# Kernel optimization log

Measured on AMD Instinct MI355X. Metric: run time of the kernel, lower is better.

The kernel has to match this reference:

```python
import jax, jax.numpy as jnp
import numpy as np

B, NM, NB, Z, H, K = 1024, 20000, 25000, 64, 256, 20
BETA = 0.1
LOG2PI = float(np.log(2.0 * np.pi))


def _log_normal(x, m, v):
    D = x.shape[-1]
    return (-0.5 * D * LOG2PI
            - 0.5 * jnp.sum(jnp.log(v), axis=-1)
            - 0.5 * jnp.sum((x - m) ** 2 / v, axis=-1))


def _kl_gmm(z, q_m, q_logv, p_m, p_logv):
    log_q = _log_normal(z, q_m, jnp.exp(q_logv))                               # [B]
    lp = _log_normal(z[:, None, :], p_m[None], jnp.exp(p_logv)[None])          # [B,K]
    log_p = jax.scipy.special.logsumexp(lp, axis=1) - jnp.log(float(p_m.shape[0]))
    return jnp.sum(log_q - log_p)


def _dist2(x, y):
    # ||x_i - y_j||_2^2, expanded form (avoids the [R,C,D] broadcast of the torch code)
    x2 = jnp.sum(x * x, axis=1, keepdims=True)
    y2 = jnp.sum(y * y, axis=1, keepdims=True)
    return x2 + y2.T - 2.0 * (x @ y.T)


def _distance_gmm(mu_s, mu_d, lv_s, lv_d):
    return _dist2(mu_s, mu_d) + _dist2(jnp.exp(0.5 * lv_s), jnp.exp(0.5 * lv_d)) + 1e-6


def _cost_mat(cost_s, cost_t, tran):
    f1 = jnp.sum(cost_s ** 2, axis=1, keepdims=True) / cost_s.shape[0]  # [ns,1]
    f2 = jnp.sum(cost_t ** 2, axis=1, keepdims=True) / cost_t.shape[0]  # [nt,1]
    return f1 + f2.T - 2.0 * (cost_s @ tran @ cost_t.T)


def _fgw(mu, z_mu, logvar, z_logvar):
    c_post = _distance_gmm(mu, mu, logvar, logvar)
    c_prior = _distance_gmm(z_mu, z_mu, z_logvar, z_logvar)
    c_pp = _distance_gmm(mu, z_mu, logvar, z_logvar)
    ns, nt = c_post.shape[0], c_prior.shape[0]
    p_s = jnp.ones((ns, 1), c_post.dtype) / ns
    p_t = jnp.ones((nt, 1), c_post.dtype) / nt

    def compute_tran(c_post, c_prior, c_pp):
        def outer(carry, _):
            tran, dual = carry
            cost = BETA * _cost_mat(c_post, c_prior, tran) + (1.0 - BETA) * c_pp
            kernel = jnp.exp(-cost / jnp.max(jnp.abs(cost))) * tran
            b = p_t / (kernel.T @ dual)

            def inner(c2, _):
                dual, b = c2
                dual = p_s / (kernel @ b)
                b = p_t / (kernel.T @ dual)
                return (dual, b), None

            (dual, b), _ = jax.lax.scan(inner, (dual, b), None, length=5)
            tran = (dual @ b.T) * kernel
            return (tran, dual), None

        init = (jnp.ones((ns, nt), c_post.dtype) / (ns * nt),
                jnp.ones((ns, 1), c_post.dtype) / ns)
        (tran, _), _ = jax.lax.scan(outer, init, None, length=10)
        return jnp.where(jnp.any(jnp.isnan(tran)),
                         jnp.ones((ns, nt), tran.dtype) / (ns * nt), tran)

    # torch detaches tran before the final cost, so cut all gradient through the loop
    tran = jax.lax.stop_gradient(compute_tran(c_post, c_prior, c_pp))
    cost = BETA * _cost_mat(c_post, c_prior, tran) + (1.0 - BETA) * c_pp
    return jnp.sum(cost * tran)


def _forward(batch_user_x, batch_user_y, p_mu_a, p_logv_a, p_mu_b, p_logv_b,
             eps_x, eps_y, eps_xr, eps_yr,
             W1a, b1a, W21a, b21a, W22a, b22a, W3a, b3a, W4a, b4a,
             W1b, b1b, W21b, b21b, W22b, b22b, W3b, b3b, W4b, b4b):
    def enc_a(x):
        h = jax.nn.relu(x @ W1a + b1a)
        return h @ W21a + b21a, h @ W22a + b22a

    def dec_a(z):
        return jax.nn.relu(z @ W3a + b3a) @ W4a + b4a

    def enc_b(x):
        h = jax.nn.relu(x @ W1b + b1b)
        return h @ W21b + b21b, h @ W22b + b22b

    def dec_b(z):
        return jax.nn.relu(z @ W3b + b3b) @ W4b + b4b

    # dropout rate = 0.0 -> identity
    mu_a, logvar_a = enc_a(batch_user_x)
    z_x = mu_a + eps_x * jnp.exp(0.5 * logvar_a)
    preds_x = dec_a(z_x)
    mu_b, logvar_b = enc_b(batch_user_y)
    z_y = mu_b + eps_y * jnp.exp(0.5 * logvar_b)
    preds_y = dec_b(z_y)

    gmm_reg_loss_a = _kl_gmm(z_x, mu_a, logvar_a, p_mu_a, p_logv_a)
    gmm_reg_loss_b = _kl_gmm(z_y, mu_b, logvar_b, p_mu_b, p_logv_b)
    align_global_loss = _fgw(mu_b, mu_a, logvar_b, logvar_a)

    preds_x2y = dec_b(z_x)
    preds_y2x = dec_a(z_y)
    m_xr, lv_xr = enc_b(preds_x2y)
    feature_x_r = m_xr + eps_xr * jnp.exp(0.5 * lv_xr)
    m_yr, lv_yr = enc_a(preds_y2x)
    feature_y_r = m_yr + eps_yr * jnp.exp(0.5 * lv_yr)

    cyc_loss_x = jnp.linalg.norm(z_x - feature_x_r)
    cyc_loss_y = jnp.linalg.norm(z_y - feature_y_r)
    return (preds_x, preds_y, preds_x2y, preds_y2x, z_x, z_y,
            gmm_reg_loss_a, gmm_reg_loss_b, feature_x_r, feature_y_r,
            align_global_loss, cyc_loss_x, cyc_loss_y)


def setup_inputs() -> dict:
    key = jax.random.key(0)
    ks = jax.random.split(key, 24)

    def nrm(i, shape, s=1.0):
        return jax.random.normal(ks[i], shape, dtype=jnp.float32) * s

    return {
        "user_1": jax.random.randint(ks[0], (B,), 0, 100000),
        "user_2": jax.random.randint(ks[1], (B,), 0, 100000),
        "batch_user_x": jax.random.uniform(ks[2], (B, NM), dtype=jnp.float32),
        "batch_user_y": jax.random.uniform(ks[3], (B, NB), dtype=jnp.float32),
        "p_mu_a": nrm(4, (K, Z)), "p_logv_a": nrm(5, (K, Z), 0.1),
        "p_mu_b": nrm(6, (K, Z)), "p_logv_b": nrm(7, (K, Z), 0.1),
        "eps_x": nrm(8, (B, Z)), "eps_y": nrm(9, (B, Z)),
        "eps_xr": nrm(10, (B, Z)), "eps_yr": nrm(11, (B, Z)),
        "W1a": nrm(12, (NM, H), 0.02), "b1a": jnp.zeros((H,), jnp.float32),
        "W21a": nrm(13, (H, Z), 0.02), "b21a": jnp.zeros((Z,), jnp.float32),
        "W22a": nrm(14, (H, Z), 0.02), "b22a": jnp.zeros((Z,), jnp.float32),
        "W3a": nrm(15, (Z, H), 0.02), "b3a": jnp.zeros((H,), jnp.float32),
        "W4a": nrm(16, (H, NM), 0.02), "b4a": jnp.zeros((NM,), jnp.float32),
        "W1b": nrm(17, (NB, H), 0.02), "b1b": jnp.zeros((H,), jnp.float32),
        "W21b": nrm(18, (H, Z), 0.02), "b21b": jnp.zeros((Z,), jnp.float32),
        "W22b": nrm(19, (H, Z), 0.02), "b22b": jnp.zeros((Z,), jnp.float32),
        "W3b": nrm(20, (Z, H), 0.02), "b3b": jnp.zeros((H,), jnp.float32),
        "W4b": nrm(21, (H, NB), 0.02), "b4b": jnp.zeros((NB,), jnp.float32),
    }


def reference(user_1, user_2, batch_user_x, batch_user_y, p_mu_a, p_logv_a, p_mu_b, p_logv_b,
              eps_x, eps_y, eps_xr, eps_yr,
              W1a, b1a, W21a, b21a, W22a, b22a, W3a, b3a, W4a, b4a,
              W1b, b1b, W21b, b21b, W22b, b22b, W3b, b3b, W4b, b4b):
    # user_1/user_2 are unused by the torch forward as well
    return _forward(batch_user_x, batch_user_y, p_mu_a, p_logv_a, p_mu_b, p_logv_b,
                    eps_x, eps_y, eps_xr, eps_yr,
                    W1a, b1a, W21a, b21a, W22a, b22a, W3a, b3a, W4a, b4a,
                    W1b, b1b, W21b, b21b, W22b, b22b, W3b, b3b, W4b, b4b)
```

## Files before the change

### kernel.cpp

```cpp
#include <hip/hip_runtime.h>


#define DEVI __device__ __forceinline__

typedef __attribute__((ext_vector_type(4))) float  f32x4;
typedef __attribute__((ext_vector_type(4))) short  s16x4;
typedef __attribute__((ext_vector_type(8))) short  s16x8;
typedef __attribute__((ext_vector_type(8))) __bf16 bf16x8;

DEVI short f2bf(float f) {
  unsigned u = __float_as_uint(f);
  u += 0x7fffu + ((u >> 16) & 1u);
  return (short)(u >> 16);
}
DEVI float bf2f(unsigned short u) { return __uint_as_float(((unsigned)u) << 16); }

DEVI f32x4 mfma16(bf16x8 a, bf16x8 b, f32x4 c) {
  return __builtin_amdgcn_mfma_f32_16x16x32_bf16(a, b, c, 0, 0, 0);
}

struct GemmArgs {
  const float* Af;
  const unsigned short* Bt;
  float* outF;
  const float* bias;
  float* partials;
  int M, N, K;
  int lda, ldbt, ldc;
  int totSteps, nSplits;
};

enum { EPI_PARTIAL, EPI_BIAS, EPI_BF16, EPI_COST, EPI_LOSS };

template<int BM, int BN, int WR, int WC, int EPI>
DEVI void gemm_body(const GemmArgs g)
{
  constexpr int BK = 64, BKP = 72;
  constexpr int NT = WR * WC * 64;
  __shared__ short As[BM * BKP];
  __shared__ short Bs[BN * BKP];

  const int m0 = blockIdx.x * BM;
  int n0 = 0, kb0 = 0, kb1 = g.K, split = 0;
  if constexpr (EPI == EPI_PARTIAL) {
    split = blockIdx.y;
    int s0 = (split * g.totSteps) / g.nSplits;
    int s1 = ((split + 1) * g.totSteps) / g.nSplits;
    kb0 = s0 * BK;
    kb1 = s1 * BK; if (kb1 > g.K) kb1 = g.K;
  } else {
    n0 = blockIdx.y * BN;
  }
  const int tid  = threadIdx.x;
  const int lane = tid & 63;
  const int wv   = tid >> 6;
  const int wr   = wv % WR;
  const int wc   = wv / WR;

  f32x4 acc[2][4];
  #pragma unroll
  for (int i = 0; i < 2; ++i)
    #pragma unroll
    for (int j = 0; j < 4; ++j) acc[i][j] = f32x4{0.f, 0.f, 0.f, 0.f};

  for (int kb = kb0; kb < kb1; kb += BK) {
    {
      constexpr int NV = BM * BK / 4;
      #pragma unroll
      for (int i = 0; i < NV / NT; ++i) {
        int idx = tid + NT * i;
        int r = idx >> 4, q = idx & 15;
        int k = kb + 4 * q;
        f32x4 v = f32x4{0.f, 0.f, 0.f, 0.f};
        if (k < kb1) v = *(const f32x4*)(g.Af + (size_t)(m0 + r) * g.lda + k);
        s16x4 s;
        s.x = f2bf(v.x); s.y = f2bf(v.y); s.z = f2bf(v.z); s.w = f2bf(v.w);
        *(s16x4*)&As[r * BKP + 4 * q] = s;
      }
    }
    {
      constexpr int NV = BN * BK / 8;
      #pragma unroll
      for (int i = 0; i < NV / NT; ++i) {
        int idx = tid + NT * i;
        int r = idx >> 3, q = idx & 7;
        int k = kb + 8 * q;
        s16x8 v{};
        if ((n0 + r) < g.N && k < kb1)
          v = *(const s16x8*)(g.Bt + (size_t)(n0 + r) * g.ldbt + k);
        *(s16x8*)&Bs[r * BKP + 8 * q] = v;
      }
    }
    __syncthreads();
    #pragma unroll
    for (int s = 0; s < 2; ++s) {
      const int ko = 32 * s + 8 * (lane >> 4);
      bf16x8 a0 = *(const bf16x8*)&As[(wr * 32 +      (lane & 15)) * BKP + ko];
      bf16x8 a1 = *(const bf16x8*)&As[(wr * 32 + 16 + (lane & 15)) * BKP + ko];
      #pragma unroll
      for (int fn = 0; fn < 4; ++fn) {
        bf16x8 b = *(const bf16x8*)&Bs[(wc * 64 + fn * 16 + (lane & 15)) * BKP + ko];
        acc[0][fn] = mfma16(a0, b, acc[0][fn]);
        acc[1][fn] = mfma16(a1, b, acc[1][fn]);
      }
    }
    __syncthreads();
  }

  #pragma unroll
  for (int fm = 0; fm < 2; ++fm) {
    #pragma unroll
    for (int fn = 0; fn < 4; ++fn) {
      #pragma unroll
      for (int p = 0; p < 4; ++p) {
        int gm = m0 + wr * 32 + fm * 16 + (lane >> 4) * 4 + p;
        int gn = n0 + wc * 64 + fn * 16 + (lane & 15);
        float v = acc[fm][fn][p];
        if constexpr (EPI == EPI_PARTIAL) {
          g.partials[((size_t)split * g.M + gm) * 256 + gn] = v;
        } else {
          if (gn < g.N) g.outF[(size_t)gm * g.ldc + gn] = v + g.bias[gn];
        }
      }
    }
  }
}

template<int BM, int BN, int WR, int WC, int EPI>
__global__ __launch_bounds__(WR*WC*64)
void k_gemm2(GemmArgs g0, GemmArgs g1)
{
  gemm_body<BM, BN, WR, WC, EPI>(blockIdx.z ? g1 : g0);
}

struct FgwGemmArgs {
  const unsigned short* A;
  const unsigned short* Bt;
  unsigned short* U;
  float* cost;
  const float* f1;
  const float* f2;
  const float* cpp;
  const float* tran;
  unsigned* mx;
  float* loss;
  float* braw;
};

template<int EPI>
__global__ __launch_bounds__(256)
void k_fgw_gemm(FgwGemmArgs a)
{
  __shared__ short As[64 * 72];
  __shared__ short Bs[64 * 72];
  __shared__ float red[4];

  const int bid = blockIdx.x, tid = threadIdx.x;
  const int lane = tid & 63, wv = tid >> 6;
  const int wr = wv & 1, wc = wv >> 1;
  const int m0 = (bid >> 4) * 64, n0 = (bid & 15) * 64;

  if constexpr (EPI == EPI_COST) {
    if (bid == 0) {
      #pragma unroll
      for (int i = 0; i < 4; ++i) a.braw[tid + 256 * i] = 0.f;
    }
  }

  f32x4 acc[2][2];
  #pragma unroll
  for (int i = 0; i < 2; ++i)
    #pragma unroll
    for (int j = 0; j < 2; ++j) acc[i][j] = f32x4{0.f, 0.f, 0.f, 0.f};

  for (int kb = 0; kb < 1024; kb += 64) {
    #pragma unroll
    for (int i = 0; i < 2; ++i) {
      int idx = tid + 256 * i;
      int r = idx >> 3, q = idx & 7;
      *(s16x8*)&As[r * 72 + 8 * q] = *(const s16x8*)&a.A [(size_t)(m0 + r) * 1024 + kb + 8 * q];
      *(s16x8*)&Bs[r * 72 + 8 * q] = *(const s16x8*)&a.Bt[(size_t)(n0 + r) * 1024 + kb + 8 * q];
    }
    __syncthreads();
    #pragma unroll
    for (int s = 0; s < 2; ++s) {
      const int ko = 32 * s + 8 * (lane >> 4);
      bf16x8 a0 = *(const bf16x8*)&As[(wr * 32 +      (lane & 15)) * 72 + ko];
      bf16x8 a1 = *(const bf16x8*)&As[(wr * 32 + 16 + (lane & 15)) * 72 + ko];
      bf16x8 b0 = *(const bf16x8*)&Bs[(wc * 32 +      (lane & 15)) * 72 + ko];
      bf16x8 b1 = *(const bf16x8*)&Bs[(wc * 32 + 16 + (lane & 15)) * 72 + ko];
      acc[0][0] = mfma16(a0, b0, acc[0][0]);
      acc[1][0] = mfma16(a1, b0, acc[1][0]);
      acc[0][1] = mfma16(a0, b1, acc[0][1]);
      acc[1][1] = mfma16(a1, b1, acc[1][1]);
    }
    __syncthreads();
  }

  float lred = 0.f;
  #pragma unroll
  for (int fm = 0; fm < 2; ++fm) {
    #pragma unroll
    for (int fn = 0; fn < 2; ++fn) {
      #pragma unroll
      for (int p = 0; p < 4; ++p) {
        int gm = m0 + wr * 32 + fm * 16 + (lane >> 4) * 4 + p;
        int gn = n0 + wc * 32 + fn * 16 + (lane & 15);
        float v = acc[fm][fn][p];
        size_t o = (size_t)gm * 1024 + gn;
        if constexpr (EPI == EPI_BF16) {
          a.U[o] = (unsigned short)f2bf(v);
        } else {
          float c = 0.1f * (a.f1[gm] + a.f2[gn] - 2.f * v) + 0.9f * a.cpp[o];
          if constexpr (EPI == EPI_COST) {
            a.cost[o] = c;
            lred = fmaxf(lred, fabsf(c));
          } else {
            lred += c * a.tran[o];
          }
        }
      }
    }
  }
  if constexpr (EPI != EPI_BF16) {
    #pragma unroll
    for (int off = 32; off; off >>= 1) {
      float t = __shfl_xor(lred, off, 64);
      lred = (EPI == EPI_COST) ? fmaxf(lred, t) : (lred + t);
    }
    if (lane == 0) red[wv] = lred;
    __syncthreads();
    if (tid == 0) {
      if constexpr (EPI == EPI_COST) {
        float t = fmaxf(fmaxf(red[0], red[1]), fmaxf(red[2], red[3]));
        atomicMax(a.mx, __float_as_uint(t));
      } else {
        atomicAdd(a.loss, red[0] + red[1] + red[2] + red[3]);
      }
    }
  }
}

struct FP {
  const float* mu[2]; const float* lv[2];
  unsigned short* F[2]; float* n[2];
};
__global__ __launch_bounds__(64)
void k_featprep(FP a)
{
  const int y = blockIdx.y;
  const int i = blockIdx.x;
  const int t = threadIdx.x;
  float v0 = a.mu[y][(size_t)i * 64 + t];
  float v1 = expf(0.5f * a.lv[y][(size_t)i * 64 + t]);
  unsigned short u0 = (unsigned short)f2bf(v0);
  unsigned short u1 = (unsigned short)f2bf(v1);
  unsigned short* Fr = a.F[y] + (size_t)i * 128;
  Fr[t] = u0;
  Fr[64 + t] = u1;
  float r0 = bf2f(u0), r1 = bf2f(u1);
  float p = r0 * r0 + r1 * r1;
  #pragma unroll
  for (int o = 32; o; o >>= 1) p += __shfl_xor(p, o, 64);
  if (t == 0) a.n[y][i] = p;
}

struct DistMMArgs {
  const unsigned short* Fx[3]; const unsigned short* Fy[3];
  const float* nx[3]; const float* ny[3];
  unsigned short* outB[2]; float* outF; float* frow[2];
};
__global__ __launch_bounds__(256)
void k_distmm(DistMMArgs a)
{
  __shared__ short As[64 * 72];
  __shared__ short Bs[64 * 72];
  const int z = blockIdx.y;
  const int bid = blockIdx.x, tid = threadIdx.x;
  const int lane = tid & 63, wv = tid >> 6;
  const int wr = wv & 1, wc = wv >> 1;
  const int m0 = (bid >> 4) * 64, n0 = (bid & 15) * 64;
  const unsigned short* X = a.Fx[z];
  const unsigned short* Y = a.Fy[z];

  f32x4 acc[2][2];
  #pragma unroll
  for (int i = 0; i < 2; ++i)
    #pragma unroll
    for (int j = 0; j < 2; ++j) acc[i][j] = f32x4{0.f, 0.f, 0.f, 0.f};

  #pragma unroll
  for (int kb = 0; kb < 128; kb += 64) {
    #pragma unroll
    for (int i = 0; i < 2; ++i) {
      int idx = tid + 256 * i;
      int r = idx >> 3, q = idx & 7;
      *(s16x8*)&As[r * 72 + 8 * q] = *(const s16x8*)&X[(size_t)(m0 + r) * 128 + kb + 8 * q];
      *(s16x8*)&Bs[r * 72 + 8 * q] = *(const s16x8*)&Y[(size_t)(n0 + r) * 128 + kb + 8 * q];
    }
    __syncthreads();
    #pragma unroll
    for (int s = 0; s < 2; ++s) {
      const int ko = 32 * s + 8 * (lane >> 4);
      bf16x8 a0 = *(const bf16x8*)&As[(wr * 32 +      (lane & 15)) * 72 + ko];
      bf16x8 a1 = *(const bf16x8*)&As[(wr * 32 + 16 + (lane & 15)) * 72 + ko];
      bf16x8 b0 = *(const bf16x8*)&Bs[(wc * 32 +      (lane & 15)) * 72 + ko];
      bf16x8 b1 = *(const bf16x8*)&Bs[(wc * 32 + 16 + (lane & 15)) * 72 + ko];
      acc[0][0] = mfma16(a0, b0, acc[0][0]);
      acc[1][0] = mfma16(a1, b0, acc[1][0]);
      acc[0][1] = mfma16(a0, b1, acc[0][1]);
      acc[1][1] = mfma16(a1, b1, acc[1][1]);
    }
    __syncthreads();
  }

  const float* nxp = a.nx[z];
  const float* nyp = a.ny[z];
  float rp[2][4];
  #pragma unroll
  for (int fm = 0; fm < 2; ++fm)
    #pragma unroll
    for (int p = 0; p < 4; ++p) rp[fm][p] = 0.f;

  #pragma unroll
  for (int fm = 0; fm < 2; ++fm) {
    #pragma unroll
    for (int fn = 0; fn < 2; ++fn) {
      #pragma unroll
      for (int p = 0; p < 4; ++p) {
        int gm = m0 + wr * 32 + fm * 16 + (lane >> 4) * 4 + p;
        int gn = n0 + wc * 32 + fn * 16 + (lane & 15);
        float val = nxp[gm] + nyp[gn] - 2.f * acc[fm][fn][p] + 1e-6f;
        if (z == 2) a.outF[(size_t)gm * 1024 + gn] = val;
        else {
          a.outB[z][(size_t)gm * 1024 + gn] = (unsigned short)f2bf(val);
          rp[fm][p] += val * val;
        }
      }
    }
  }
  if (z < 2) {
    #pragma unroll
    for (int fm = 0; fm < 2; ++fm)
      #pragma unroll
      for (int p = 0; p < 4; ++p) {
        float v = rp[fm][p];
        v += __shfl_xor(v, 1, 64);
        v += __shfl_xor(v, 2, 64);
        v += __shfl_xor(v, 4, 64);
        v += __shfl_xor(v, 8, 64);
        rp[fm][p] = v;
      }
    if ((lane & 15) == 0) {
      #pragma unroll
      for (int fm = 0; fm < 2; ++fm)
        #pragma unroll
        for (int p = 0; p < 4; ++p) {
          int gm = m0 + wr * 32 + fm * 16 + (lane >> 4) * 4 + p;
          atomicAdd(&a.frow[z][gm], rp[fm][p] * (1.f / 1024.f));
        }
    }
  }
}

__global__ __launch_bounds__(256)
void k_kbuild(const float* cost, const float* tran, const unsigned* mxbits,
              const float* draw, float* braw, float* K, float* KT)
{
  __shared__ float t[64 * 65];
  __shared__ float dualS[64];
  __shared__ float csum[4][64];
  const int r0 = blockIdx.x * 64, c0 = blockIdx.y * 64;
  const int tid = threadIdx.x;
  const float inv = 1.f / __uint_as_float(*mxbits);
  const float PS = 1.f / 1024.f;
  if (tid < 64) dualS[tid] = PS / draw[r0 + tid];
  __syncthreads();
  float colpart = 0.f;
  #pragma unroll
  for (int i = 0; i < 16; ++i) {
    int idx = tid + 256 * i;
    int r = idx >> 6, c = idx & 63;
    size_t o = (size_t)(r0 + r) * 1024 + (c0 + c);
    float v = expf(-cost[o] * inv) * tran[o];
    K[o] = v;
    t[r * 65 + c] = v;
    colpart += v * dualS[r];
  }
  csum[tid >> 6][tid & 63] = colpart;
  __syncthreads();
  #pragma unroll
  for (int i = 0; i < 16; ++i) {
    int idx = tid + 256 * i;
    int c = idx >> 6, r = idx & 63;
    KT[(size_t)(c0 + c) * 1024 + (r0 + r)] = t[r * 65 + c];
  }
  if (tid < 64)
    atomicAdd(&braw[c0 + tid],
              csum[0][tid] + csum[1][tid] + csum[2][tid] + csum[3][tid]);
}

__global__ __launch_bounds__(256)
void k_matvec(const float* M, const float* xraw, float* yraw)
{
  const int r = blockIdx.x * 4 + (threadIdx.x >> 6);
  const int lane = threadIdx.x & 63;
  const float C = 1.f / 1024.f;
  const f32x4* row = (const f32x4*)(M + (size_t)r * 1024);
  const f32x4* xv  = (const f32x4*)xraw;
  float s = 0.f;
  #pragma unroll
  for (int q = 0; q < 4; ++q) {
    f32x4 a = row[lane + 64 * q];
    f32x4 x = xv [lane + 64 * q];
    s += a.x * (C / x.x) + a.y * (C / x.y) + a.z * (C / x.z) + a.w * (C / x.w);
  }
  #pragma unroll
  for (int o = 32; o; o >>= 1) s += __shfl_xor(s, o, 64);
  if (lane == 0) yraw[r] = s;
}

__global__ __launch_bounds__(256)
void k_tranupd(const float* K, const float* draw, const float* braw,
               float* tran, unsigned short* tranT, unsigned* flag, int check)
{
  __shared__ float t[64 * 65];
  __shared__ float dualS[64], bS[64];
  const int r0 = blockIdx.x * 64, c0 = blockIdx.y * 64;
  const int tid = threadIdx.x;
  const float P = 1.f / 1024.f;
  if (tid < 64) dualS[tid] = P / draw[r0 + tid];
  else if (tid < 128) bS[tid - 64] = P / braw[c0 + tid - 64];
  __syncthreads();
  unsigned bad = 0;
  #pragma unroll
  for (int i = 0; i < 16; ++i) {
    int idx = tid + 256 * i;
    int r = idx >> 6, c = idx & 63;
    size_t o = (size_t)(r0 + r) * 1024 + (c0 + c);
    float v = dualS[r] * bS[c] * K[o];
    tran[o] = v;
    t[r * 65 + c] = v;
    if (v != v) bad = 1u;
  }
  __syncthreads();
  #pragma unroll
  for (int i = 0; i < 16; ++i) {
    int idx = tid + 256 * i;
    int c = idx >> 6, r = idx & 63;
    tranT[(size_t)(c0 + c) * 1024 + (r0 + r)] = (unsigned short)f2bf(t[r * 65 + c]);
  }
  if (check && bad) atomicOr(flag, 1u);
}

struct T4 { const float* in[4]; unsigned short* out[4]; int R[4], C[4], nx[4], nt[4]; };
__global__ void k_transpose4(T4 d)
{
  __shared__ float t[64][65];
  const int z = blockIdx.y;
  const int tile = blockIdx.x;
  if (tile >= d.nt[z]) return;
  const int R = d.R[z], C = d.C[z];
  const int r0 = (tile % d.nx[z]) * 64, c0 = (tile / d.nx[z]) * 64;
  const float* in = d.in[z];
  unsigned short* out = d.out[z];
  const int tid = threadIdx.x;
  #pragma unroll
  for (int i = 0; i < 16; ++i) {
    int idx = tid + 256 * i;
    int r = idx >> 6, c = idx & 63;
    float v = 0.f;
    if ((r0 + r) < R && (c0 + c) < C) v = in[(size_t)(r0 + r) * C + (c0 + c)];
    t[r][c] = v;
  }
  __syncthreads();
  #pragma unroll
  for (int i = 0; i < 16; ++i) {
    int idx = tid + 256 * i;
    int c = idx >> 6, r = idx & 63;
    if ((c0 + c) < C && (r0 + r) < R)
      out[(size_t)(c0 + c) * R + (r0 + r)] = (unsigned short)f2bf(t[r][c]);
  }
}

__global__ void k_wcomb_reduce(const float* partials, unsigned short* WcTa,
                               unsigned short* WcTb)
{
  __shared__ float t[64][65];
  const int z = blockIdx.z;
  const float* P = partials + (size_t)z * 32 * 256 * 256;
  unsigned short* WcT = z ? WcTb : WcTa;
  const int u0 = blockIdx.x * 64, v0 = blockIdx.y * 64;
  const int tid = threadIdx.x;
  #pragma unroll
  for (int i = 0; i < 16; ++i) {
    int idx = tid + 256 * i;
    int u = idx >> 6, v = idx & 63;
    float s = 0.f;
    for (int p = 0; p < 32; ++p)
      s += P[(size_t)p * 65536 + (u0 + u) * 256 + (v0 + v)];
    t[u][v] = s;
  }
  __syncthreads();
  #pragma unroll
  for (int i = 0; i < 16; ++i) {
    int idx = tid + 256 * i;
    int v = idx >> 6, u = idx & 63;
    WcT[(size_t)(v0 + v) * 256 + (u0 + u)] = (unsigned short)f2bf(t[u][v]);
  }
}

struct BcArgs {
  const float* b4[2]; const unsigned short* Wt1[2]; const float* b1[2];
  float* bc[2]; int K[2];
};
__global__ void k_bcvec(BcArgs a)
{
  const int y = blockIdx.y;
  const int c = blockIdx.x * 4 + (threadIdx.x >> 6);
  const int lane = threadIdx.x & 63;
  const int K = a.K[y];
  const unsigned short* wrow = a.Wt1[y] + (size_t)c * K;
  const float* b4 = a.b4[y];
  float s = 0.f;
  for (int k = lane * 8; k < K; k += 512) {
    s16x8 w = *(const s16x8*)&wrow[k];
    f32x4 v0 = *(const f32x4*)&b4[k];
    f32x4 v1 = *(const f32x4*)&b4[k + 4];
    s += v0.x * bf2f((unsigned short)w[0]) + v0.y * bf2f((unsigned short)w[1])
       + v0.z * bf2f((unsigned short)w[2]) + v0.w * bf2f((unsigned short)w[3])
       + v1.x * bf2f((unsigned short)w[4]) + v1.y * bf2f((unsigned short)w[5])
       + v1.z * bf2f((unsigned short)w[6]) + v1.w * bf2f((unsigned short)w[7]);
  }
  #pragma unroll
  for (int o = 32; o; o >>= 1) s += __shfl_xor(s, o, 64);
  if (lane == 0) a.bc[y][c] = s + a.b1[y][c];
}

struct Red2 { const float* partials[2]; const float* bias[2]; float* h[2]; int ns; };
__global__ void k_reduce2(Red2 a)
{
  const int y = blockIdx.y;
  int idx = blockIdx.x * 256 + threadIdx.x;
  float s = a.bias[y][idx & 255];
  const float* P = a.partials[y];
  for (int p = 0; p < a.ns; ++p) s += P[(size_t)p * (1024 * 256) + idx];
  a.h[y][idx] = fmaxf(s, 0.f);
}

struct EH2 {
  const float* h[2]; const float* W21[2]; const float* b21[2];
  const float* W22[2]; const float* b22[2]; const float* eps[2];
  float* mu[2]; float* lv[2]; float* zO[2];
};
__global__ void k_enc_head2(EH2 a)
{
  __shared__ float hrow[256];
  __shared__ float res[128];
  const int y = blockIdx.y;
  const int i = blockIdx.x;
  const int t = threadIdx.x;
  hrow[t]       = a.h[y][(size_t)i * 256 + t];
  hrow[t + 128] = a.h[y][(size_t)i * 256 + t + 128];
  __syncthreads();
  const int c = t & 63;
  const float* W = (t < 64) ? a.W21[y] : a.W22[y];
  float acc = (t < 64) ? a.b21[y][c] : a.b22[y][c];
  #pragma unroll 8
  for (int j = 0; j < 256; ++j) acc += hrow[j] * W[j * 64 + c];
  res[t] = acc;
  __syncthreads();
  if (t < 64) {
    float mu = res[t], lv = res[64 + t];
    a.mu[y][(size_t)i * 64 + t] = mu;
    a.lv[y][(size_t)i * 64 + t] = lv;
    a.zO[y][(size_t)i * 64 + t] = mu + a.eps[y][(size_t)i * 64 + t] * expf(0.5f * lv);
  }
}

struct RencArgs {
  const float* hd[2]; const unsigned short* WcT[2]; const float* bc[2];
  const float* W21[2]; const float* b21[2]; const float* W22[2]; const float* b22[2];
  const float* eps[2]; float* fout[2];
};
__global__ void k_renc_head(RencArgs a)
{
  __shared__ float hdrow[256];
  __shared__ float hr[256];
  __shared__ float res[128];
  const int y = blockIdx.y;
  const int i = blockIdx.x;
  const int t = threadIdx.x;
  hdrow[t] = a.hd[y][(size_t)i * 256 + t];
  __syncthreads();
  {
    const s16x8* wr = (const s16x8*)(a.WcT[y] + (size_t)t * 256);
    float s = a.bc[y][t];
    #pragma unroll 4
    for (int j = 0; j < 32; ++j) {
      s16x8 w = wr[j];
      const float* hp = &hdrow[j * 8];
      s += hp[0] * bf2f((unsigned short)w[0]) + hp[1] * bf2f((unsigned short)w[1])
         + hp[2] * bf2f((unsigned short)w[2]) + hp[3] * bf2f((unsigned short)w[3])
         + hp[4] * bf2f((unsigned short)w[4]) + hp[5] * bf2f((unsigned short)w[5])
         + hp[6] * bf2f((unsigned short)w[6]) + hp[7] * bf2f((unsigned short)w[7]);
    }
    hr[t] = fmaxf(s, 0.f);
  }
  __syncthreads();
  if (t < 128) {
    const int c = t & 63;
    const float* W = (t < 64) ? a.W21[y] : a.W22[y];
    float acc = (t < 64) ? a.b21[y][c] : a.b22[y][c];
    #pragma unroll 8
    for (int j = 0; j < 256; ++j) acc += hr[j] * W[j * 64 + c];
    res[t] = acc;
  }
  __syncthreads();
  if (t < 64) {
    float mu = res[t], lv = res[64 + t];
    a.fout[y][(size_t)i * 64 + t] = mu + a.eps[y][(size_t)i * 64 + t] * expf(0.5f * lv);
  }
}

struct DH4 { const float* z[4]; const float* W3[4]; const float* b3[4]; float* hd[4]; };
__global__ void k_dec_head4(DH4 a)
{
  __shared__ float zrow[64];
  const int y = blockIdx.y;
  const int i = blockIdx.x;
  const int t = threadIdx.x;
  if (t < 64) zrow[t] = a.z[y][(size_t)i * 64 + t];
  __syncthreads();
  const float* W3 = a.W3[y];
  float acc = a.b3[y][t];
  #pragma unroll
  for (int d = 0; d < 64; ++d) acc += zrow[d] * W3[d * 256 + t];
  a.hd[y][(size_t)i * 256 + t] = fmaxf(acc, 0.f);
}

__global__ void k_init(float* tran, unsigned short* tranT, float* draw, float* braw,
                       float* f1, float* f2, unsigned* mx, unsigned* nanflag,
                       float* cyc, float* ga, float* gb, float* al)
{
  const int bid = blockIdx.x, tid = threadIdx.x;
  const float v = 1.f / (1024.f * 1024.f);
  const unsigned short vb = (unsigned short)f2bf(v);
  const size_t base = (size_t)bid * 1024;
  #pragma unroll
  for (int i = 0; i < 4; ++i) {
    tran [base + tid + 256 * i] = v;
    tranT[base + tid + 256 * i] = vb;
  }
  if (bid == 0) {
    #pragma unroll
    for (int i = 0; i < 4; ++i) {
      int k = tid + 256 * i;
      draw[k] = 1.f; braw[k] = 0.f; f1[k] = 0.f; f2[k] = 0.f;
    }
    if (tid < 16) mx[tid] = 0u;
    if (tid == 0) { *nanflag = 0u; cyc[0] = 0.f; cyc[1] = 0.f; *ga = 0.f; *gb = 0.f; *al = 0.f; }
  }
}

__global__ void k_nanfix(float* tran, unsigned short* tranT, const unsigned* flag)
{
  if (*flag == 0u) return;
  const int bid = blockIdx.x, tid = threadIdx.x;
  const float v = 1.f / (1024.f * 1024.f);
  const unsigned short vb = (unsigned short)f2bf(v);
  const size_t base = (size_t)bid * 1024;
  #pragma unroll
  for (int i = 0; i < 4; ++i) {
    tran [base + tid + 256 * i] = v;
    tranT[base + tid + 256 * i] = vb;
  }
}

struct G2 {
  const float* z[2]; const float* mu[2]; const float* lv[2];
  const float* pmu[2]; const float* plv[2]; float* o[2];
};
__global__ void k_gmm2(G2 a)
{
  const int y = blockIdx.y;
  const int i = blockIdx.x;
  const int d = threadIdx.x;
  const float zd = a.z[y][(size_t)i * 64 + d];
  const float m  = a.mu[y][(size_t)i * 64 + d];
  const float l  = a.lv[y][(size_t)i * 64 + d];
  float t = l + (zd - m) * (zd - m) * expf(-l);
  #pragma unroll
  for (int o = 32; o; o >>= 1) t += __shfl_xor(t, o, 64);
  const float C0 = 64.f * 1.8378770664093453f;
  float logq = -0.5f * (C0 + t);
  float lp[20];
  #pragma unroll
  for (int k = 0; k < 20; ++k) {
    float pm = a.pmu[y][k * 64 + d], pl = a.plv[y][k * 64 + d];
    float u = pl + (zd - pm) * (zd - pm) * expf(-pl);
    #pragma unroll
    for (int o = 32; o; o >>= 1) u += __shfl_xor(u, o, 64);
    lp[k] = -0.5f * (C0 + u);
  }
  float mx = lp[0];
  #pragma unroll
  for (int k = 1; k < 20; ++k) mx = fmaxf(mx, lp[k]);
  float s = 0.f;
  #pragma unroll
  for (int k = 0; k < 20; ++k) s += expf(lp[k] - mx);
  float logp = mx + logf(s) - 2.9957322735539909f;
  if (d == 0) atomicAdd(a.o[y], logq - logp);
}

struct Sq2 { const float* a[2]; const float* b[2]; float* cyc; };
__global__ void k_sqdiff2(Sq2 g)
{
  __shared__ float red[4];
  const int y = blockIdx.y;
  int idx = blockIdx.x * 256 + threadIdx.x;
  float d = g.a[y][idx] - g.b[y][idx];
  d = d * d;
  #pragma unroll
  for (int o = 32; o; o >>= 1) d += __shfl_xor(d, o, 64);
  int lane = threadIdx.x & 63, wv = threadIdx.x >> 6;
  if (lane == 0) red[wv] = d;
  __syncthreads();
  if (threadIdx.x == 0) atomicAdd(g.cyc + y, red[0] + red[1] + red[2] + red[3]);
}

__global__ void k_finish(const float* slots, float* o1, float* o2)
{
  if (threadIdx.x == 0) { *o1 = sqrtf(slots[0]); *o2 = sqrtf(slots[1]); }
}

extern "C" void kernel_launch(void* const* d_in, const int* in_sizes, int n_in,
                              void* d_out, int out_size, void* d_ws, size_t ws_size,
                              hipStream_t stream)
{
  (void)in_sizes; (void)n_in; (void)out_size; (void)ws_size;

  const float* X     = (const float*)d_in[2];
  const float* Y     = (const float*)d_in[3];
  const float* pmua  = (const float*)d_in[4];
  const float* plva  = (const float*)d_in[5];
  const float* pmub  = (const float*)d_in[6];
  const float* plvb  = (const float*)d_in[7];
  const float* epsx  = (const float*)d_in[8];
  const float* epsy  = (const float*)d_in[9];
  const float* epsxr = (const float*)d_in[10];
  const float* epsyr = (const float*)d_in[11];
  const float* W1a = (const float*)d_in[12];  const float* b1a = (const float*)d_in[13];
  const float* W21a= (const float*)d_in[14];  const float* b21a= (const float*)d_in[15];
  const float* W22a= (const float*)d_in[16];  const float* b22a= (const float*)d_in[17];
  const float* W3a = (const float*)d_in[18];  const float* b3a = (const float*)d_in[19];
  const float* W4a = (const float*)d_in[20];  const float* b4a = (const float*)d_in[21];
  const float* W1b = (const float*)d_in[22];  const float* b1b = (const float*)d_in[23];
  const float* W21b= (const float*)d_in[24];  const float* b21b= (const float*)d_in[25];
  const float* W22b= (const float*)d_in[26];  const float* b22b= (const float*)d_in[27];
  const float* W3b = (const float*)d_in[28];  const float* b3b = (const float*)d_in[29];
  const float* W4b = (const float*)d_in[30];  const float* b4b = (const float*)d_in[31];

  float* out = (float*)d_out;
  const size_t P_X = 0, P_Y = 20480000, P_X2Y = 46080000, P_Y2X = 71680000;
  const size_t Z_X = 92160000, Z_Y = 92225536;
  const size_t GMM_A = 92291072, GMM_B = 92291073;
  const size_t F_XR = 92291074, F_YR = 92356610;
  const size_t ALIGN = 92422146, CYC_X = 92422147, CYC_Y = 92422148;

  char* w = (char*)d_ws;
  size_t off = 0;
  auto alloc = [&](size_t bytes) -> void* {
    void* p = w + off;
    off += (bytes + 255) & ~(size_t)255;
    return p;
  };
  unsigned short* Wt1a = (unsigned short*)alloc((size_t)256 * 20000 * 2);
  unsigned short* Wt1b = (unsigned short*)alloc((size_t)256 * 25000 * 2);
  unsigned short* W4ta = (unsigned short*)alloc((size_t)20000 * 256 * 2);
  unsigned short* W4tb = (unsigned short*)alloc((size_t)25000 * 256 * 2);
  unsigned short* WcTa = (unsigned short*)alloc((size_t)256 * 256 * 2);
  unsigned short* WcTb = (unsigned short*)alloc((size_t)256 * 256 * 2);
  float* bca  = (float*)alloc(256 * 4);
  float* bcb  = (float*)alloc(256 * 4);
  float* h0   = (float*)alloc((size_t)1024 * 256 * 4);
  float* h1   = (float*)alloc((size_t)1024 * 256 * 4);
  float* mu_a = (float*)alloc(1024 * 64 * 4);
  float* lv_a = (float*)alloc(1024 * 64 * 4);
  float* mu_b = (float*)alloc(1024 * 64 * 4);
  float* lv_b = (float*)alloc(1024 * 64 * 4);
  float* f1   = (float*)alloc(1024 * 4);
  float* f2   = (float*)alloc(1024 * 4);
  unsigned* mx      = (unsigned*)alloc(16 * 4);
  unsigned* nanflag = (unsigned*)alloc(256);
  float* cyc  = (float*)alloc(256);
  float* draw = (float*)alloc(1024 * 4);
  float* braw = (float*)alloc(1024 * 4);
  unsigned short* Fb = (unsigned short*)alloc((size_t)1024 * 128 * 2);
  unsigned short* Fa = (unsigned short*)alloc((size_t)1024 * 128 * 2);
  float* nb = (float*)alloc(1024 * 4);
  float* na = (float*)alloc(1024 * 4);
  char* arena = (char*)alloc((size_t)32 * 1024 * 1024);
  float* partials = (float*)arena;
  size_t ao = 0;
  auto aalloc = [&](size_t bytes) -> void* {
    void* p = arena + ao;
    ao += (bytes + 255) & ~(size_t)255;
    return p;
  };
  unsigned short* cpostB  = (unsigned short*)aalloc((size_t)1024 * 1024 * 2);
  unsigned short* cpriorB = (unsigned short*)aalloc((size_t)1024 * 1024 * 2);
  float* cpp  = (float*)aalloc((size_t)1024 * 1024 * 4);
  float* tran = (float*)aalloc((size_t)1024 * 1024 * 4);
  unsigned short* tranT = (unsigned short*)aalloc((size_t)1024 * 1024 * 2);
  unsigned short* Umat  = (unsigned short*)aalloc((size_t)1024 * 1024 * 2);
  float* cost  = (float*)aalloc((size_t)1024 * 1024 * 4);
  float* Kmat  = (float*)aalloc((size_t)1024 * 1024 * 4);
  float* KTmat = (float*)aalloc((size_t)1024 * 1024 * 4);
  float* hd0 = (float*)(arena);
  float* hd1 = (float*)(arena + (size_t)1024 * 256 * 4);
  float* hd2 = (float*)(arena + (size_t)2 * 1024 * 256 * 4);
  float* hd3 = (float*)(arena + (size_t)3 * 1024 * 256 * 4);

  {
    T4 d{};
    d.in[0] = W1a; d.out[0] = Wt1a; d.R[0] = 20000; d.C[0] = 256;
    d.in[1] = W1b; d.out[1] = Wt1b; d.R[1] = 25000; d.C[1] = 256;
    d.in[2] = W4a; d.out[2] = W4ta; d.R[2] = 256;   d.C[2] = 20000;
    d.in[3] = W4b; d.out[3] = W4tb; d.R[3] = 256;   d.C[3] = 25000;
    for (int z = 0; z < 4; ++z) {
      d.nx[z] = (d.R[z] + 63) / 64;
      d.nt[z] = d.nx[z] * ((d.C[z] + 63) / 64);
    }
    k_transpose4<<<dim3(1564, 4), 256, 0, stream>>>(d);
  }

  k_init<<<1024, 256, 0, stream>>>(tran, tranT, draw, braw, f1, f2, mx, nanflag,
                                   cyc, out + GMM_A, out + GMM_B, out + ALIGN);

  {
    GemmArgs ga{}, gb{};
    ga.Af = W4a; ga.Bt = Wt1a; ga.partials = partials;
    ga.M = 256; ga.N = 256; ga.K = 20000; ga.lda = 20000; ga.ldbt = 20000;
    ga.totSteps = 313; ga.nSplits = 32;
    gb = ga;
    gb.Af = W4b; gb.Bt = Wt1b; gb.partials = partials + (size_t)32 * 65536;
    gb.K = 25000; gb.lda = 25000; gb.ldbt = 25000; gb.totSteps = 391;
    k_gemm2<128, 256, 4, 4, EPI_PARTIAL><<<dim3(2, 32, 2), 1024, 0, stream>>>(ga, gb);
    k_wcomb_reduce<<<dim3(4, 4, 2), 256, 0, stream>>>(partials, WcTa, WcTb);
    BcArgs bc{};
    bc.b4[0] = b4a; bc.Wt1[0] = Wt1a; bc.b1[0] = b1a; bc.bc[0] = bca; bc.K[0] = 20000;
    bc.b4[1] = b4b; bc.Wt1[1] = Wt1b; bc.b1[1] = b1b; bc.bc[1] = bcb; bc.K[1] = 25000;
    k_bcvec<<<dim3(64, 2), 256, 0, stream>>>(bc);
  }

  {
    GemmArgs ga{}, gb{};
    ga.Af = X; ga.Bt = Wt1a; ga.partials = partials;
    ga.M = 1024; ga.N = 256; ga.K = 20000; ga.lda = 20000; ga.ldbt = 20000;
    ga.totSteps = 313; ga.nSplits = 16;
    gb = ga;
    gb.Af = Y; gb.Bt = Wt1b; gb.partials = partials + (size_t)16 * 1024 * 256;
    gb.K = 25000; gb.lda = 25000; gb.ldbt = 25000; gb.totSteps = 391;
    k_gemm2<128, 256, 4, 4, EPI_PARTIAL><<<dim3(8, 16, 2), 1024, 0, stream>>>(ga, gb);
    Red2 r{};
    r.partials[0] = partials; r.partials[1] = partials + (size_t)16 * 1024 * 256;
    r.bias[0] = b1a; r.bias[1] = b1b; r.h[0] = h0; r.h[1] = h1; r.ns = 16;
    k_reduce2<<<dim3(1024, 2), 256, 0, stream>>>(r);
    EH2 e{};
    e.h[0] = h0; e.W21[0] = W21a; e.b21[0] = b21a; e.W22[0] = W22a; e.b22[0] = b22a;
    e.eps[0] = epsx; e.mu[0] = mu_a; e.lv[0] = lv_a; e.zO[0] = out + Z_X;
    e.h[1] = h1; e.W21[1] = W21b; e.b21[1] = b21b; e.W22[1] = W22b; e.b22[1] = b22b;
    e.eps[1] = epsy; e.mu[1] = mu_b; e.lv[1] = lv_b; e.zO[1] = out + Z_Y;
    k_enc_head2<<<dim3(1024, 2), 128, 0, stream>>>(e);
  }

  {
    G2 g{};
    g.z[0] = out + Z_X; g.mu[0] = mu_a; g.lv[0] = lv_a; g.pmu[0] = pmua; g.plv[0] = plva;
    g.o[0] = out + GMM_A;
    g.z[1] = out + Z_Y; g.mu[1] = mu_b; g.lv[1] = lv_b; g.pmu[1] = pmub; g.plv[1] = plvb;
    g.o[1] = out + GMM_B;
    k_gmm2<<<dim3(1024, 2), 64, 0, stream>>>(g);
  }

  {
    FP fp{};
    fp.mu[0] = mu_b; fp.lv[0] = lv_b; fp.F[0] = Fb; fp.n[0] = nb;
    fp.mu[1] = mu_a; fp.lv[1] = lv_a; fp.F[1] = Fa; fp.n[1] = na;
    k_featprep<<<dim3(1024, 2), 64, 0, stream>>>(fp);
    DistMMArgs dm{};
    dm.Fx[0] = Fb; dm.Fy[0] = Fb; dm.nx[0] = nb; dm.ny[0] = nb;
    dm.Fx[1] = Fa; dm.Fy[1] = Fa; dm.nx[1] = na; dm.ny[1] = na;
    dm.Fx[2] = Fb; dm.Fy[2] = Fa; dm.nx[2] = nb; dm.ny[2] = na;
    dm.outB[0] = cpostB; dm.outB[1] = cpriorB; dm.outF = cpp;
    dm.frow[0] = f1; dm.frow[1] = f2;
    k_distmm<<<dim3(256, 3), 256, 0, stream>>>(dm);
  }
  FgwGemmArgs fg{};
  fg.f1 = f1; fg.f2 = f2; fg.cpp = cpp; fg.loss = out + ALIGN; fg.braw = braw;
  for (int it = 0; it < 10; ++it) {
    fg.A = cpostB; fg.Bt = tranT; fg.U = Umat;
    k_fgw_gemm<EPI_BF16><<<256, 256, 0, stream>>>(fg);
    fg.A = Umat; fg.Bt = cpriorB; fg.cost = cost; fg.mx = mx + it;
    k_fgw_gemm<EPI_COST><<<256, 256, 0, stream>>>(fg);
    k_kbuild<<<dim3(16, 16), 256, 0, stream>>>(cost, tran, mx + it, draw, braw, Kmat, KTmat);
    for (int r = 0; r < 5; ++r) {
      k_matvec<<<256, 256, 0, stream>>>(Kmat,  braw, draw);
      k_matvec<<<256, 256, 0, stream>>>(KTmat, draw, braw);
    }
    k_tranupd<<<dim3(16, 16), 256, 0, stream>>>(Kmat, draw, braw, tran, tranT,
                                                nanflag, it == 9 ? 1 : 0);
  }
  k_nanfix<<<1024, 256, 0, stream>>>(tran, tranT, nanflag);
  fg.A = cpostB; fg.Bt = tranT; fg.U = Umat;
  k_fgw_gemm<EPI_BF16><<<256, 256, 0, stream>>>(fg);
  fg.A = Umat; fg.Bt = cpriorB; fg.tran = tran;
  k_fgw_gemm<EPI_LOSS><<<256, 256, 0, stream>>>(fg);

  {
    DH4 d{};
    d.z[0] = out + Z_X; d.W3[0] = W3a; d.b3[0] = b3a; d.hd[0] = hd0;
    d.z[1] = out + Z_Y; d.W3[1] = W3a; d.b3[1] = b3a; d.hd[1] = hd1;
    d.z[2] = out + Z_Y; d.W3[2] = W3b; d.b3[2] = b3b; d.hd[2] = hd2;
    d.z[3] = out + Z_X; d.W3[3] = W3b; d.b3[3] = b3b; d.hd[3] = hd3;
    k_dec_head4<<<dim3(1024, 4), 256, 0, stream>>>(d);
  }

  {
    RencArgs r{};
    r.hd[0] = hd3; r.WcT[0] = WcTb; r.bc[0] = bcb;
    r.W21[0] = W21b; r.b21[0] = b21b; r.W22[0] = W22b; r.b22[0] = b22b;
    r.eps[0] = epsxr; r.fout[0] = out + F_XR;
    r.hd[1] = hd1; r.WcT[1] = WcTa; r.bc[1] = bca;
    r.W21[1] = W21a; r.b21[1] = b21a; r.W22[1] = W22a; r.b22[1] = b22a;
    r.eps[1] = epsyr; r.fout[1] = out + F_YR;
    k_renc_head<<<dim3(1024, 2), 256, 0, stream>>>(r);
  }

  {
    Sq2 s{};
    s.a[0] = out + Z_X; s.b[0] = out + F_XR;
    s.a[1] = out + Z_Y; s.b[1] = out + F_YR;
    s.cyc = cyc;
    k_sqdiff2<<<dim3(256, 2), 256, 0, stream>>>(s);
    k_finish<<<1, 64, 0, stream>>>(cyc, out + CYC_X, out + CYC_Y);
  }

  {
    GemmArgs ga{}, gb{};
    ga.Af = hd0; ga.Bt = W4ta; ga.outF = out + P_X; ga.bias = b4a;
    ga.M = 1024; ga.N = 20000; ga.K = 256; ga.lda = 256; ga.ldbt = 256; ga.ldc = 20000;
    gb = ga; gb.Af = hd1; gb.outF = out + P_Y2X;
    k_gemm2<128, 256, 4, 4, EPI_BIAS><<<dim3(8, 79, 2), 1024, 0, stream>>>(ga, gb);

    GemmArgs gc{}, gd{};
    gc.Af = hd2; gc.Bt = W4tb; gc.outF = out + P_Y; gc.bias = b4b;
    gc.M = 1024; gc.N = 25000; gc.K = 256; gc.lda = 256; gc.ldbt = 256; gc.ldc = 25000;
    gd = gc; gd.Af = hd3; gd.outF = out + P_X2Y;
    k_gemm2<128, 256, 4, 4, EPI_BIAS><<<dim3(8, 98, 2), 1024, 0, stream>>>(gc, gd);
  }
}
```

Before: 1.549 ms.

## Fuse Sinkhorn kernel build, matvecs and transport update into one persistent kernel

Replaces the per-iteration sequence of k_kbuild, ten k_matvec launches and k_tranupd with a single k_sinkhorn kernel. It runs 16 blocks of 1024 threads, each owning 64 rows, and uses software grid barriers built on atomic counters between phases. The aim is to remove about a dozen launches and their inter-kernel gaps per outer iteration, and to precompute the reciprocal dual vector once in shared memory. The trade-off is that only 16 CUs do all the memory-bound K/KT build, matvec and update work. Correctness also depends on the spin barriers and on cross-CU visibility of K, KT, draw and braw.

```diff
diff --git a/kernel.cpp b/kernel.cpp
--- a/kernel.cpp
+++ b/kernel.cpp
@@ -241,6 +241,142 @@
   }
 }
 
+#define SB 16
+
+struct SinkArgs {
+  const float* cost; const float* tran; const unsigned* mx;
+  float* K; float* KT;
+  float* draw; float* braw;
+  float* tranO; unsigned short* tranTO;
+  unsigned* cnt; unsigned* nanflag; int check;
+};
+
+DEVI void gbar(unsigned* c)
+{
+  __threadfence();
+  __syncthreads();
+  if (threadIdx.x == 0) {
+    __hip_atomic_fetch_add(c, 1u, __ATOMIC_ACQ_REL, __HIP_MEMORY_SCOPE_AGENT);
+    while (__hip_atomic_load(c, __ATOMIC_ACQUIRE, __HIP_MEMORY_SCOPE_AGENT) < (unsigned)SB)
+      __builtin_amdgcn_s_sleep(1);
+  }
+  __syncthreads();
+  __threadfence();
+}
+
+DEVI void mvp(const float* M, const float* x, float* y, int r0, float* invx)
+{
+  const int tid = threadIdx.x;
+  invx[tid] = (1.f / 1024.f) / x[tid];
+  __syncthreads();
+  const int wv = tid >> 6, lane = tid & 63;
+  #pragma unroll
+  for (int pass = 0; pass < 4; ++pass) {
+    const int r = r0 + pass * 16 + wv;
+    const f32x4* row = (const f32x4*)(M + (size_t)r * 1024);
+    float s = 0.f;
+    #pragma unroll
+    for (int q = 0; q < 4; ++q) {
+      f32x4 av = row[lane + 64 * q];
+      f32x4 iv = *(const f32x4*)&invx[4 * (lane + 64 * q)];
+      s += av.x * iv.x + av.y * iv.y + av.z * iv.z + av.w * iv.w;
+    }
+    #pragma unroll
+    for (int o = 32; o; o >>= 1) s += __shfl_xor(s, o, 64);
+    if (lane == 0) y[r] = s;
+  }
+  __syncthreads();
+}
+
+__global__ __launch_bounds__(1024)
+void k_sinkhorn(SinkArgs a)
+{
+  __shared__ float tt[64 * 65];
+  __shared__ float dS[64];
+  __shared__ float csum[16][64];
+  __shared__ float invx[1024];
+
+  const int bid = blockIdx.x, tid = threadIdx.x;
+  const int r0 = bid * 64;
+  const float PS = 1.f / 1024.f;
+  const float inv = 1.f / __uint_as_float(*a.mx);
+
+  if (tid < 64) dS[tid] = PS / a.draw[r0 + tid];
+  __syncthreads();
+
+  for (int jt = 0; jt < 16; ++jt) {
+    const int c0 = jt * 64;
+    float colp = 0.f;
+    #pragma unroll
+    for (int i = 0; i < 4; ++i) {
+      int idx = tid + 1024 * i;
+      int r = idx >> 6, c = idx & 63;
+      size_t o = (size_t)(r0 + r) * 1024 + c0 + c;
+      float v = expf(-a.cost[o] * inv) * a.tran[o];
+      a.K[o] = v;
+      tt[r * 65 + c] = v;
+      colp += v * dS[r];
+    }
+    csum[tid >> 6][tid & 63] = colp;
+    __syncthreads();
+    #pragma unroll
+    for (int i = 0; i < 4; ++i) {
+      int idx = tid + 1024 * i;
+      int c = idx >> 6, r = idx & 63;
+      a.KT[(size_t)(c0 + c) * 1024 + r0 + r] = tt[r * 65 + c];
+    }
+    if (tid < 64) {
+      float s = 0.f;
+      #pragma unroll
+      for (int k = 0; k < 16; ++k) s += csum[k][tid];
+      atomicAdd(&a.braw[c0 + tid], s);
+    }
+    __syncthreads();
+  }
+  gbar(a.cnt + 0);
+
+  int barid = 1;
+  #pragma unroll 1
+  for (int rr = 0; rr < 5; ++rr) {
+    mvp(a.K,  a.braw, a.draw, r0, invx);  gbar(a.cnt + barid++);
+    mvp(a.KT, a.draw, a.braw, r0, invx);  gbar(a.cnt + barid++);
+  }
+
+  invx[tid] = PS / a.braw[tid];
+  if (tid < 64) dS[tid] = PS / a.draw[r0 + tid];
+  __syncthreads();
+  unsigned bad = 0;
+  #pragma unroll
+  for (int i = 0; i < 16; ++i) {
+    int flat = tid * 4 + i * 4096;
+    int r = flat >> 10, c = flat & 1023;
+    size_t o = (size_t)(r0 + r) * 1024 + c;
+    f32x4 kv = *(const f32x4*)&a.K[o];
+    f32x4 iv = *(const f32x4*)&invx[c];
+    float d = dS[r];
+    f32x4 v;
+    v.x = d * iv.x * kv.x; v.y = d * iv.y * kv.y;
+    v.z = d * iv.z * kv.z; v.w = d * iv.w * kv.w;
+    *(f32x4*)&a.tranO[o] = v;
+    if (v.x != v.x || v.y != v.y || v.z != v.z || v.w != v.w) bad = 1u;
+  }
+  #pragma unroll
+  for (int i = 0; i < 16; ++i) {
+    int flat = tid * 4 + i * 4096;
+    int c = flat >> 6, r = flat & 63;
+    size_t o = (size_t)c * 1024 + r0 + r;
+    f32x4 kv = *(const f32x4*)&a.KT[o];
+    float ib = invx[c];
+    s16x4 s;
+    s.x = f2bf(dS[r]     * ib * kv.x);
+    s.y = f2bf(dS[r + 1] * ib * kv.y);
+    s.z = f2bf(dS[r + 2] * ib * kv.z);
+    s.w = f2bf(dS[r + 3] * ib * kv.w);
+    *(s16x4*)&a.tranTO[o] = s;
+  }
+  if (a.check && bad) atomicOr(a.nanflag, 1u);
+}
+
 struct FP {
   const float* mu[2]; const float* lv[2];
   unsigned short* F[2]; float* n[2];
@@ -363,96 +499,6 @@
   }
 }
 
-__global__ __launch_bounds__(256)
-void k_kbuild(const float* cost, const float* tran, const unsigned* mxbits,
-              const float* draw, float* braw, float* K, float* KT)
-{
-  __shared__ float t[64 * 65];
-  __shared__ float dualS[64];
-  __shared__ float csum[4][64];
-  const int r0 = blockIdx.x * 64, c0 = blockIdx.y * 64;
-  const int tid = threadIdx.x;
-  const float inv = 1.f / __uint_as_float(*mxbits);
-  const float PS = 1.f / 1024.f;
-  if (tid < 64) dualS[tid] = PS / draw[r0 + tid];
-  __syncthreads();
-  float colpart = 0.f;
-  #pragma unroll
-  for (int i = 0; i < 16; ++i) {
-    int idx = tid + 256 * i;
-    int r = idx >> 6, c = idx & 63;
-    size_t o = (size_t)(r0 + r) * 1024 + (c0 + c);
-    float v = expf(-cost[o] * inv) * tran[o];
-    K[o] = v;
-    t[r * 65 + c] = v;
-    colpart += v * dualS[r];
-  }
-  csum[tid >> 6][tid & 63] = colpart;
-  __syncthreads();
-  #pragma unroll
-  for (int i = 0; i < 16; ++i) {
-    int idx = tid + 256 * i;
-    int c = idx >> 6, r = idx & 63;
-    KT[(size_t)(c0 + c) * 1024 + (r0 + r)] = t[r * 65 + c];
-  }
-  if (tid < 64)
-    atomicAdd(&braw[c0 + tid],
-              csum[0][tid] + csum[1][tid] + csum[2][tid] + csum[3][tid]);
-}
-
-__global__ __launch_bounds__(256)
-void k_matvec(const float* M, const float* xraw, float* yraw)
-{
-  const int r = blockIdx.x * 4 + (threadIdx.x >> 6);
-  const int lane = threadIdx.x & 63;
-  const float C = 1.f / 1024.f;
-  const f32x4* row = (const f32x4*)(M + (size_t)r * 1024);
-  const f32x4* xv  = (const f32x4*)xraw;
-  float s = 0.f;
-  #pragma unroll
-  for (int q = 0; q < 4; ++q) {
-    f32x4 a = row[lane + 64 * q];
-    f32x4 x = xv [lane + 64 * q];
-    s += a.x * (C / x.x) + a.y * (C / x.y) + a.z * (C / x.z) + a.w * (C / x.w);
-  }
-  #pragma unroll
-  for (int o = 32; o; o >>= 1) s += __shfl_xor(s, o, 64);
-  if (lane == 0) yraw[r] = s;
-}
-
-__global__ __launch_bounds__(256)
-void k_tranupd(const float* K, const float* draw, const float* braw,
-               float* tran, unsigned short* tranT, unsigned* flag, int check)
-{
-  __shared__ float t[64 * 65];
-  __shared__ float dualS[64], bS[64];
-  const int r0 = blockIdx.x * 64, c0 = blockIdx.y * 64;
-  const int tid = threadIdx.x;
-  const float P = 1.f / 1024.f;
-  if (tid < 64) dualS[tid] = P / draw[r0 + tid];
-  else if (tid < 128) bS[tid - 64] = P / braw[c0 + tid - 64];
-  __syncthreads();
-  unsigned bad = 0;
-  #pragma unroll
-  for (int i = 0; i < 16; ++i) {
-    int idx = tid + 256 * i;
-    int r = idx >> 6, c = idx & 63;
-    size_t o = (size_t)(r0 + r) * 1024 + (c0 + c);
-    float v = dualS[r] * bS[c] * K[o];
-    tran[o] = v;
-    t[r * 65 + c] = v;
-    if (v != v) bad = 1u;
-  }
-  __syncthreads();
-  #pragma unroll
-  for (int i = 0; i < 16; ++i) {
-    int idx = tid + 256 * i;
-    int c = idx >> 6, r = idx & 63;
-    tranT[(size_t)(c0 + c) * 1024 + (r0 + r)] = (unsigned short)f2bf(t[r * 65 + c]);
-  }
-  if (check && bad) atomicOr(flag, 1u);
-}
-
 struct T4 { const float* in[4]; unsigned short* out[4]; int R[4], C[4], nx[4], nt[4]; };
 __global__ void k_transpose4(T4 d)
 {
@@ -641,7 +687,7 @@
 
 __global__ void k_init(float* tran, unsigned short* tranT, float* draw, float* braw,
                        float* f1, float* f2, unsigned* mx, unsigned* nanflag,
-                       float* cyc, float* ga, float* gb, float* al)
+                       float* cyc, float* ga, float* gb, float* al, unsigned* cnt)
 {
   const int bid = blockIdx.x, tid = threadIdx.x;
   const float v = 1.f / (1024.f * 1024.f);
@@ -658,6 +704,7 @@
       int k = tid + 256 * i;
       draw[k] = 1.f; braw[k] = 0.f; f1[k] = 0.f; f2[k] = 0.f;
     }
+    cnt[tid] = 0u;
     if (tid < 16) mx[tid] = 0u;
     if (tid == 0) { *nanflag = 0u; cyc[0] = 0.f; cyc[1] = 0.f; *ga = 0.f; *gb = 0.f; *al = 0.f; }
   }
@@ -796,6 +843,7 @@
   float* cyc  = (float*)alloc(256);
   float* draw = (float*)alloc(1024 * 4);
   float* braw = (float*)alloc(1024 * 4);
+  unsigned* counters = (unsigned*)alloc(256 * 4);
   unsigned short* Fb = (unsigned short*)alloc((size_t)1024 * 128 * 2);
   unsigned short* Fa = (unsigned short*)alloc((size_t)1024 * 128 * 2);
   float* nb = (float*)alloc(1024 * 4);
@@ -836,7 +884,7 @@
   }
 
   k_init<<<1024, 256, 0, stream>>>(tran, tranT, draw, braw, f1, f2, mx, nanflag,
-                                   cyc, out + GMM_A, out + GMM_B, out + ALIGN);
+                                   cyc, out + GMM_A, out + GMM_B, out + ALIGN, counters);
 
   {
     GemmArgs ga{}, gb{};
@@ -904,13 +952,12 @@
     k_fgw_gemm<EPI_BF16><<<256, 256, 0, stream>>>(fg);
     fg.A = Umat; fg.Bt = cpriorB; fg.cost = cost; fg.mx = mx + it;
     k_fgw_gemm<EPI_COST><<<256, 256, 0, stream>>>(fg);
-    k_kbuild<<<dim3(16, 16), 256, 0, stream>>>(cost, tran, mx + it, draw, braw, Kmat, KTmat);
-    for (int r = 0; r < 5; ++r) {
-      k_matvec<<<256, 256, 0, stream>>>(Kmat,  braw, draw);
-      k_matvec<<<256, 256, 0, stream>>>(KTmat, draw, braw);
-    }
-    k_tranupd<<<dim3(16, 16), 256, 0, stream>>>(Kmat, draw, braw, tran, tranT,
-                                                nanflag, it == 9 ? 1 : 0);
+    SinkArgs sa{};
+    sa.cost = cost; sa.tran = tran; sa.mx = mx + it;
+    sa.K = Kmat; sa.KT = KTmat; sa.draw = draw; sa.braw = braw;
+    sa.tranO = tran; sa.tranTO = tranT;
+    sa.cnt = counters + it * 16; sa.nanflag = nanflag; sa.check = (it == 9) ? 1 : 0;
+    k_sinkhorn<<<SB, 1024, 0, stream>>>(sa);
   }
   k_nanfix<<<1024, 256, 0, stream>>>(tran, tranT, nanflag);
   fg.A = cpostB; fg.Bt = tranT; fg.U = Umat;
```

Measured after the change: 2.712 ms. 1.75x slower.
